# Performance work log

Measured on AMD Instinct MI355X. Metric: run time of the kernel, lower is better.

Reference implementation:

```python
import jax, jax.numpy as jnp
import numpy as np

N_TH1 = 30
LB = 1e-20
UB = 1e20
LB_EXP = -20.0
UB_EXP = 20.0


def make_directions(n_th1):
    # Reproduces the TF __init__ direction sampling on the sphere.
    n_th2 = 2 * (n_th1 - 1) + 1
    th1 = np.linspace(-np.pi / 2, np.pi / 2, n_th1)
    th2 = np.linspace(-np.pi, np.pi, n_th2)
    c1, s1 = np.cos(th1), np.sin(th1)
    c2, s2 = np.cos(th2), np.sin(th2)
    dx = np.outer(c1[1:-1], c2[:-1])          # [n_th1-2, n_th2-1]
    dy = np.outer(c1[1:-1], s2[:-1])
    dz = np.broadcast_to(s1[1:-1, None], dx.shape)
    mid = np.stack([dx, dy, dz], -1).reshape(-1, 3)
    poles = np.array([[c1[0] * c2[0], c1[0] * s2[0], s1[0]],
                      [c1[-1] * c2[0], c1[-1] * s2[0], s1[-1]]])
    return np.concatenate([mid, poles], 0).astype(np.float32)  # [D, 3]


def setup_inputs() -> dict:
    key = jax.random.key(0)
    k1, k2, k3 = jax.random.split(key, 3)
    vertices = jax.random.normal(k1, (8, 64, 32, 3), jnp.float32)
    # smoothness is a p-norm exponent; realistic range [2, 20]
    smoothness = 2.0 + 18.0 * jax.random.uniform(k2, (8, 64), jnp.float32)
    pointcloud = jax.random.normal(k3, (8, 2048, 3), jnp.float32)
    return {"vertices": vertices, "smoothness": smoothness, "pointcloud": pointcloud}


def _spt_forward(vertices, smoothness):
    dirs = jnp.asarray(make_directions(N_TH1))            # [D, 3]
    B, P = vertices.shape[0], vertices.shape[1]
    mean_v = jnp.mean(vertices, axis=2, keepdims=True)    # [B,P,1,3]
    local_v = vertices - mean_v                           # [B,P,V,3]

    # z = <v, x> for every vertex/direction pair -> [B,P,V,D]
    z = jnp.einsum('bpvc,dc->bpvd', local_v, dirs)
    zm = jnp.maximum(z, 0.0)
    p = smoothness[:, :, None, None]                      # [B,P,1,1]

    # dynamic rescaling k = 10^ceil(...) to keep zm^p in fp range
    zm_max = jnp.max(zm, axis=2, keepdims=True)           # [B,P,1,D]
    zm_log = jnp.log(zm_max) / jnp.log(10.0)              # = max over V of log10(zm)
    exponent = zm_log * p
    lk = jnp.where(exponent < LB_EXP, (-15.0 - exponent) / p, 0.0)
    k = 10.0 ** jnp.clip(jnp.ceil(lk), 0.0, UB_EXP)       # [B,P,1,D]
    k = jax.lax.stop_gradient(k)                          # ceil has zero grad anyway

    zm = zm * k
    pos = zm > 0
    # clip(zm^p, lb, ub) - (zm==0)*lb  ==  where(zm>0, clip(zm^p,lb,ub), 0)
    zm_p = jnp.where(pos, jnp.clip(jnp.where(pos, zm, 1.0) ** p, LB, UB), 0.0)
    sum_zm_p = jnp.sum(zm_p, axis=2, keepdims=True)       # [B,P,1,D]
    spos = sum_zm_p > 0
    h = jnp.where(spos, jnp.clip(jnp.where(spos, sum_zm_p, 1.0) ** (1.0 / p), LB, UB), LB)

    # dh/dz = clip((zm/h)^(p-1), lb, ub)
    ratio = zm / h                                        # [B,P,V,D]
    rpos = ratio > 0
    dhdz = jnp.where(rpos, jnp.clip(jnp.where(rpos, ratio, 1.0) ** (p - 1.0), LB, UB), LB)
    # dh/dx = dhdz^T @ vertices -> surface points
    dhdx = jnp.einsum('bpvd,bpvc->bpdc', dhdz, local_v)   # [B,P,D,3]
    surf = dhdx + mean_v                                  # broadcast [B,P,1,3]

    h_out = jnp.clip(h / k, -UB, UB)                      # [B,P,1,D]
    h_out = jnp.transpose(h_out, (0, 1, 3, 2))            # [B,P,D,1]
    local_dirs = jnp.broadcast_to(dirs[None, None], (B, P) + dirs.shape)
    direction_h = jnp.concatenate([local_dirs, h_out], axis=-1)  # [B,P,D,4]
    points = surf.reshape(B, -1, 3)                       # [B, P*D, 3]
    mean_out = mean_v.reshape(B, P, 3)
    return points, direction_h, mean_out, local_v


def reference(vertices, smoothness, pointcloud):
    points, direction_h, mean_out, local_v = _spt_forward(vertices, smoothness)
    B, P = vertices.shape[0], vertices.shape[1]
    # overlap / retraction loops are truncated in the source; placeholders
    overlap = jnp.zeros((B, P, 1), jnp.float32)
    retraction = jnp.zeros((B, P, 1), jnp.float32)
    return (points, direction_h, overlap, retraction, mean_out, local_v)
```

## Files before the change

### kernel.cpp

```cpp
#include <hip/hip_runtime.h>
#include <math.h>

#define NBP 512
#define VV 32
#define DD 1626
#define CHUNKS 4
#define DPC 407

#define O_POINTS 0
#define O_DIRH   2497536
#define O_OVER   5827584
#define O_RETR   5828096
#define O_MEAN   5828608
#define O_LOCAL  5830144

#define L10_2 0.3010299956639812f
#define L2_10 3.321928094887362f
#define LH_MIN -66.43856189774725f

__device__ __forceinline__ void make_dir(int d, float& x, float& y, float& z) {
  if (d < 1624) {
    int i1 = d / 58;
    int i2 = d - i1 * 58;
    i1 += 1;
    const float STEP = 0.10833078115826873f;
    float th1 = -1.5707963267948966f + (float)i1 * STEP;
    float th2 = -3.14159265358979323846f + (float)i2 * STEP;
    float s1, c1, s2, c2;
    sincosf(th1, &s1, &c1);
    sincosf(th2, &s2, &c2);
    x = c1 * c2; y = c1 * s2; z = s1;
  } else if (d == 1624) {
    x = -6.123234e-17f; y = -7.49880e-33f; z = -1.0f;
  } else {
    x = -6.123234e-17f; y = -7.49880e-33f; z = 1.0f;
  }
}

__global__ __launch_bounds__(256) void dirs_kernel(float* __restrict__ gdirs) {
  int d = blockIdx.x * 256 + threadIdx.x;
  if (d >= DD) return;
  float x, y, z;
  make_dir(d, x, y, z);
  gdirs[d * 3 + 0] = x;
  gdirs[d * 3 + 1] = y;
  gdirs[d * 3 + 2] = z;
}

__global__ __launch_bounds__(256) void spt_kernel(
    const float* __restrict__ vertices,
    const float* __restrict__ smooth,
    const float* __restrict__ gdirs,
    float* __restrict__ out)
{
  const int bp    = blockIdx.x;
  const int chunk = blockIdx.y;
  const int tid   = threadIdx.x;

  __shared__ float vb[VV * 3];
  __shared__ float lv[VV * 3];
  __shared__ float meanv[3];
  __shared__ float sdir[DPC * 3];

  if (tid < VV * 3) vb[tid] = vertices[bp * (VV * 3) + tid];

  const int dbase = chunk * DPC;
  const int dend  = (DD - dbase) < DPC ? (DD - dbase) : DPC;

  if (gdirs) {
    for (int i = tid; i < dend * 3; i += 256) sdir[i] = gdirs[dbase * 3 + i];
  } else {
    for (int i = tid; i < dend; i += 256) {
      float x, y, z;
      make_dir(dbase + i, x, y, z);
      sdir[i * 3 + 0] = x; sdir[i * 3 + 1] = y; sdir[i * 3 + 2] = z;
    }
  }
  __syncthreads();

  if (tid < 3) {
    float s = 0.f;
#pragma unroll
    for (int v = 0; v < VV; v++) s += vb[v * 3 + tid];
    meanv[tid] = s * (1.0f / 32.0f);
  }
  __syncthreads();
  if (tid < VV * 3) lv[tid] = vb[tid] - meanv[tid % 3];
  __syncthreads();

  if (chunk == 0) {
    if (tid < VV * 3) out[O_LOCAL + bp * (VV * 3) + tid] = lv[tid];
    if (tid < 3)      out[O_MEAN + bp * 3 + tid] = meanv[tid];
    if (tid == 3)     out[O_OVER + bp] = 0.f;
    if (tid == 4)     out[O_RETR + bp] = 0.f;
  }

  const float p     = smooth[bp];
  const float inv_p = 1.0f / p;
  const float pm1   = p - 1.0f;
  const float mx = meanv[0], my = meanv[1], mz = meanv[2];

  for (int i = tid; i < dend; i += 256) {
    const int d = dbase + i;
    const float dx = sdir[i * 3 + 0];
    const float dy = sdir[i * 3 + 1];
    const float dz = sdir[i * 3 + 2];

    float lz[VV];
    float zmax = 0.f;
#pragma unroll
    for (int v = 0; v < VV; v++) {
      float zv = fmaf(lv[v * 3 + 0], dx,
                  fmaf(lv[v * 3 + 1], dy, lv[v * 3 + 2] * dz));
      zv = fmaxf(zv, 0.f);
      zmax = fmaxf(zmax, zv);
      lz[v] = __log2f(zv);
    }

    const float expo = __log2f(zmax) * (p * L10_2);
    float kc = 0.f;
    if (expo < -20.f) {
      kc = fminf(fmaxf(ceilf((-15.f - expo) * inv_p), 0.f), 20.f);
    }
    const float kcl = kc * L2_10;
    const float pkc = p * kcl;

    float ssum = 0.f;
#pragma unroll
    for (int v = 0; v < VV; v++) {
      float zp = exp2f(fmaf(p, lz[v], pkc));
      zp = fminf(zp, 1e20f);
      ssum += zp;
    }

    float lh = LH_MIN;
    if (ssum > 0.f) lh = inv_p * __log2f(ssum);

    const float c3 = pm1 * (kcl - lh);
    float ax = 0.f, ay = 0.f, az = 0.f;
#pragma unroll
    for (int v = 0; v < VV; v++) {
      float dh = exp2f(fmaf(pm1, lz[v], c3));
      dh = fminf(dh, 1e20f);
      ax = fmaf(dh, lv[v * 3 + 0], ax);
      ay = fmaf(dh, lv[v * 3 + 1], ay);
      az = fmaf(dh, lv[v * 3 + 2], az);
    }

    const int pbase = bp * DD + d;
    out[O_POINTS + pbase * 3 + 0] = ax + mx;
    out[O_POINTS + pbase * 3 + 1] = ay + my;
    out[O_POINTS + pbase * 3 + 2] = az + mz;

    const float hout = exp2f(lh - kcl);
    out[O_DIRH + pbase * 4 + 0] = dx;
    out[O_DIRH + pbase * 4 + 1] = dy;
    out[O_DIRH + pbase * 4 + 2] = dz;
    out[O_DIRH + pbase * 4 + 3] = hout;
  }
}

extern "C" void kernel_launch(void* const* d_in, const int* in_sizes, int n_in,
                              void* d_out, int out_size, void* d_ws, size_t ws_size,
                              hipStream_t stream) {
  const float* vertices = (const float*)d_in[0];
  const float* smooth   = (const float*)d_in[1];
  float* out = (float*)d_out;

  const size_t dirs_bytes = (size_t)DD * 3 * sizeof(float);
  float* gdirs = (ws_size >= dirs_bytes) ? (float*)d_ws : nullptr;

  if (gdirs) {
    dirs_kernel<<<dim3((DD + 255) / 256), 256, 0, stream>>>(gdirs);
  }
  spt_kernel<<<dim3(NBP, CHUNKS), 256, 0, stream>>>(vertices, smooth, gdirs, out);
}
```

Baseline: 92.84 us.

## Use one direction per thread across seven tiles with SoA vertex layout

```diff
diff --git a/kernel.cpp b/kernel.cpp
--- a/kernel.cpp
+++ b/kernel.cpp
@@ -4,8 +4,8 @@
 #define NBP 512
 #define VV 32
 #define DD 1626
-#define CHUNKS 4
-#define DPC 407
+#define TILE 256
+#define NTILES 7
 
 #define O_POINTS 0
 #define O_DIRH   2497536
@@ -17,6 +17,10 @@
 #define L10_2 0.3010299956639812f
 #define L2_10 3.321928094887362f
 #define LH_MIN -66.43856189774725f
+
+__device__ __forceinline__ float fexp2(float x) {
+  return __builtin_amdgcn_exp2f(x);
+}
 
 __device__ __forceinline__ void make_dir(int d, float& x, float& y, float& z) {
   if (d < 1624) {
@@ -54,27 +58,24 @@
     float* __restrict__ out)
 {
   const int bp    = blockIdx.x;
-  const int chunk = blockIdx.y;
+  const int tile  = blockIdx.y;
   const int tid   = threadIdx.x;
 
   __shared__ float vb[VV * 3];
-  __shared__ float lv[VV * 3];
+  __shared__ __align__(16) float slvx[VV];
+  __shared__ __align__(16) float slvy[VV];
+  __shared__ __align__(16) float slvz[VV];
   __shared__ float meanv[3];
-  __shared__ float sdir[DPC * 3];
+  __shared__ __align__(16) float4 sdir[TILE];
 
   if (tid < VV * 3) vb[tid] = vertices[bp * (VV * 3) + tid];
 
-  const int dbase = chunk * DPC;
-  const int dend  = (DD - dbase) < DPC ? (DD - dbase) : DPC;
+  const int dbase = tile * TILE;
+  const int dend  = (DD - dbase) < TILE ? (DD - dbase) : TILE;
 
-  if (gdirs) {
-    for (int i = tid; i < dend * 3; i += 256) sdir[i] = gdirs[dbase * 3 + i];
-  } else {
-    for (int i = tid; i < dend; i += 256) {
-      float x, y, z;
-      make_dir(dbase + i, x, y, z);
-      sdir[i * 3 + 0] = x; sdir[i * 3 + 1] = y; sdir[i * 3 + 2] = z;
-    }
+  if (tid < dend) {
+    const float* g = gdirs + (size_t)(dbase + tid) * 3;
+    sdir[tid] = make_float4(g[0], g[1], g[2], 0.f);
   }
   __syncthreads();
 
@@ -85,79 +86,93 @@
     meanv[tid] = s * (1.0f / 32.0f);
   }
   __syncthreads();
-  if (tid < VV * 3) lv[tid] = vb[tid] - meanv[tid % 3];
+  if (tid < VV) {
+    slvx[tid] = vb[tid * 3 + 0] - meanv[0];
+    slvy[tid] = vb[tid * 3 + 1] - meanv[1];
+    slvz[tid] = vb[tid * 3 + 2] - meanv[2];
+  }
   __syncthreads();
 
-  if (chunk == 0) {
-    if (tid < VV * 3) out[O_LOCAL + bp * (VV * 3) + tid] = lv[tid];
+  if (tile == 0) {
+    if (tid < VV * 3) out[O_LOCAL + bp * (VV * 3) + tid] = vb[tid] - meanv[tid % 3];
     if (tid < 3)      out[O_MEAN + bp * 3 + tid] = meanv[tid];
     if (tid == 3)     out[O_OVER + bp] = 0.f;
     if (tid == 4)     out[O_RETR + bp] = 0.f;
   }
+
+  if (tid >= dend) return;
 
   const float p     = smooth[bp];
   const float inv_p = 1.0f / p;
   const float pm1   = p - 1.0f;
   const float mx = meanv[0], my = meanv[1], mz = meanv[2];
 
-  for (int i = tid; i < dend; i += 256) {
-    const int d = dbase + i;
-    const float dx = sdir[i * 3 + 0];
-    const float dy = sdir[i * 3 + 1];
-    const float dz = sdir[i * 3 + 2];
+  float4 dv = sdir[tid];
+  const float dx = dv.x, dy = dv.y, dz = dv.z;
+  const int d = dbase + tid;
 
-    float lz[VV];
-    float zmax = 0.f;
+  const float4* lvx4 = (const float4*)slvx;
+  const float4* lvy4 = (const float4*)slvy;
+  const float4* lvz4 = (const float4*)slvz;
+
+  float lz[VV];
+  float lmax = -INFINITY;
 #pragma unroll
-    for (int v = 0; v < VV; v++) {
-      float zv = fmaf(lv[v * 3 + 0], dx,
-                  fmaf(lv[v * 3 + 1], dy, lv[v * 3 + 2] * dz));
-      zv = fmaxf(zv, 0.f);
-      zmax = fmaxf(zmax, zv);
-      lz[v] = __log2f(zv);
-    }
+  for (int j = 0; j < VV / 4; j++) {
+    float4 X = lvx4[j], Y = lvy4[j], Z = lvz4[j];
+    float z0 = fmaxf(fmaf(X.x, dx, fmaf(Y.x, dy, Z.x * dz)), 0.f);
+    float z1 = fmaxf(fmaf(X.y, dx, fmaf(Y.y, dy, Z.y * dz)), 0.f);
+    float z2 = fmaxf(fmaf(X.z, dx, fmaf(Y.z, dy, Z.z * dz)), 0.f);
+    float z3 = fmaxf(fmaf(X.w, dx, fmaf(Y.w, dy, Z.w * dz)), 0.f);
+    float l0 = __log2f(z0), l1 = __log2f(z1);
+    float l2 = __log2f(z2), l3 = __log2f(z3);
+    lz[j * 4 + 0] = l0; lz[j * 4 + 1] = l1;
+    lz[j * 4 + 2] = l2; lz[j * 4 + 3] = l3;
+    lmax = fmaxf(lmax, fmaxf(fmaxf(l0, l1), fmaxf(l2, l3)));
+  }
 
-    const float expo = __log2f(zmax) * (p * L10_2);
-    float kc = 0.f;
-    if (expo < -20.f) {
-      kc = fminf(fmaxf(ceilf((-15.f - expo) * inv_p), 0.f), 20.f);
-    }
-    const float kcl = kc * L2_10;
-    const float pkc = p * kcl;
+  const float expo = lmax * (p * L10_2);
+  float kc = 0.f;
+  if (expo < -20.f) {
+    kc = fminf(fmaxf(ceilf((-15.f - expo) * inv_p), 0.f), 20.f);
+  }
+  const float kcl = kc * L2_10;
+  const float pkc = p * kcl;
 
-    float ssum = 0.f;
+  float s0 = 0.f, s1 = 0.f, s2 = 0.f, s3 = 0.f;
 #pragma unroll
-    for (int v = 0; v < VV; v++) {
-      float zp = exp2f(fmaf(p, lz[v], pkc));
-      zp = fminf(zp, 1e20f);
-      ssum += zp;
-    }
+  for (int j = 0; j < VV / 4; j++) {
+    s0 += fminf(fexp2(fmaf(p, lz[j * 4 + 0], pkc)), 1e20f);
+    s1 += fminf(fexp2(fmaf(p, lz[j * 4 + 1], pkc)), 1e20f);
+    s2 += fminf(fexp2(fmaf(p, lz[j * 4 + 2], pkc)), 1e20f);
+    s3 += fminf(fexp2(fmaf(p, lz[j * 4 + 3], pkc)), 1e20f);
+  }
+  const float ssum = (s0 + s1) + (s2 + s3);
 
-    float lh = LH_MIN;
-    if (ssum > 0.f) lh = inv_p * __log2f(ssum);
+  float lh = LH_MIN;
+  if (ssum > 0.f) lh = inv_p * __log2f(ssum);
 
-    const float c3 = pm1 * (kcl - lh);
-    float ax = 0.f, ay = 0.f, az = 0.f;
+  const float c3 = pm1 * (kcl - lh);
+  float ax = 0.f, ay = 0.f, az = 0.f;
 #pragma unroll
-    for (int v = 0; v < VV; v++) {
-      float dh = exp2f(fmaf(pm1, lz[v], c3));
-      dh = fminf(dh, 1e20f);
-      ax = fmaf(dh, lv[v * 3 + 0], ax);
-      ay = fmaf(dh, lv[v * 3 + 1], ay);
-      az = fmaf(dh, lv[v * 3 + 2], az);
-    }
+  for (int j = 0; j < VV / 4; j++) {
+    float4 X = lvx4[j], Y = lvy4[j], Z = lvz4[j];
+    float d0 = fminf(fexp2(fmaf(pm1, lz[j * 4 + 0], c3)), 1e20f);
+    float d1 = fminf(fexp2(fmaf(pm1, lz[j * 4 + 1], c3)), 1e20f);
+    float d2 = fminf(fexp2(fmaf(pm1, lz[j * 4 + 2], c3)), 1e20f);
+    float d3 = fminf(fexp2(fmaf(pm1, lz[j * 4 + 3], c3)), 1e20f);
+    ax = fmaf(d0, X.x, fmaf(d1, X.y, fmaf(d2, X.z, fmaf(d3, X.w, ax))));
+    ay = fmaf(d0, Y.x, fmaf(d1, Y.y, fmaf(d2, Y.z, fmaf(d3, Y.w, ay))));
+    az = fmaf(d0, Z.x, fmaf(d1, Z.y, fmaf(d2, Z.z, fmaf(d3, Z.w, az))));
+  }
 
-    const int pbase = bp * DD + d;
-    out[O_POINTS + pbase * 3 + 0] = ax + mx;
-    out[O_POINTS + pbase * 3 + 1] = ay + my;
-    out[O_POINTS + pbase * 3 + 2] = az + mz;
+  const int pbase = bp * DD + d;
+  out[O_POINTS + pbase * 3 + 0] = ax + mx;
+  out[O_POINTS + pbase * 3 + 1] = ay + my;
+  out[O_POINTS + pbase * 3 + 2] = az + mz;
 
-    const float hout = exp2f(lh - kcl);
-    out[O_DIRH + pbase * 4 + 0] = dx;
-    out[O_DIRH + pbase * 4 + 1] = dy;
-    out[O_DIRH + pbase * 4 + 2] = dz;
-    out[O_DIRH + pbase * 4 + 3] = hout;
-  }
+  dv.w = fexp2(lh - kcl);
+  ((float4*)(out + O_DIRH))[pbase] = dv;
 }
 
 extern "C" void kernel_launch(void* const* d_in, const int* in_sizes, int n_in,
@@ -166,12 +181,8 @@
   const float* vertices = (const float*)d_in[0];
   const float* smooth   = (const float*)d_in[1];
   float* out = (float*)d_out;
+  float* gdirs = (float*)d_ws;
 
-  const size_t dirs_bytes = (size_t)DD * 3 * sizeof(float);
-  float* gdirs = (ws_size >= dirs_bytes) ? (float*)d_ws : nullptr;
-
-  if (gdirs) {
-    dirs_kernel<<<dim3((DD + 255) / 256), 256, 0, stream>>>(gdirs);
-  }
-  spt_kernel<<<dim3(NBP, CHUNKS), 256, 0, stream>>>(vertices, smooth, gdirs, out);
+  dirs_kernel<<<dim3((DD + 255) / 256), 256, 0, stream>>>(gdirs);
+  spt_kernel<<<dim3(NBP, NTILES), 256, 0, stream>>>(vertices, smooth, gdirs, out);
 }
```

New measurement: 80.51 us. 13.3% less time.
